# Optimization experiments

Measured on AMD Instinct MI355X. Metric: run time of the kernel, lower is better.

## Reference

```python
import jax, jax.numpy as jnp
import numpy as np

DEPTH_PARAM = 0.5
LENGTH_PENALTY = 1.5
LEVEL_COUNTS = [8, 32, 128, 512, 2048]  # nodes per tree level (branching factor 4)
BRANCH = 4
B = 4096


def _build_tree():
    counts = LEVEL_COUNTS
    D = len(counts)
    offsets = np.concatenate([[0], np.cumsum(counts)]).astype(np.int64)
    C = int(offsets[-1])
    path_ids = np.zeros((C, D), np.int32)   # ancestor matrix-id at each level (0-padded)
    path_len = np.zeros((C,), np.int32)     # depth of this class (= len of its path)
    sib_start = np.zeros((C, D), np.int32)  # start of contiguous sibling block at each level
    sib_size = np.zeros((C, D), np.int32)   # size of that block (valid_classes in torch code)
    for l in range(D):
        for k in range(counts[l]):
            gid = offsets[l] + k
            path_len[gid] = l + 1
            kk = k
            for a in range(l, -1, -1):
                path_ids[gid, a] = offsets[a] + kk
                if a == 0:
                    sib_start[gid, a] = 0
                    sib_size[gid, a] = counts[0]
                else:
                    sib_start[gid, a] = offsets[a] + (kk // BRANCH) * BRANCH
                    sib_size[gid, a] = BRANCH
                kk = kk // BRANCH
    return path_ids, path_len, sib_start, sib_size, C


def setup_inputs() -> dict:
    path_ids, path_len, sib_start, sib_size, C = _build_tree()
    key = jax.random.key(0)
    k1, k2 = jax.random.split(key)
    y_pred = jax.random.normal(k1, (B, C), dtype=jnp.float32)
    y_true = jax.random.normal(k2, (B, C), dtype=jnp.float32)  # only argmax is used
    rng = np.random.default_rng(0)
    counts = rng.integers(1, 1000, size=C).astype(np.float32)
    class_weights = jnp.asarray(counts.max() / counts, dtype=jnp.float32)
    return {
        "y_pred": y_pred,
        "y_true": y_true,
        "class_weights": class_weights,
        "path_ids": jnp.asarray(path_ids),
        "path_len": jnp.asarray(path_len),
        "sib_start": jnp.asarray(sib_start),
        "sib_size": jnp.asarray(sib_size),
    }


def reference(y_pred, y_true, class_weights, path_ids, path_len, sib_start, sib_size):
    Bsz, C = y_pred.shape
    D = path_ids.shape[1]
    pred_top = jnp.argmax(y_pred, axis=1)                    # [B]
    true_top = jnp.argmax(y_true, axis=1)                    # [B]
    len_p = path_len[pred_top]                               # [B]
    len_t = path_len[true_top]                               # [B]
    levels = jnp.arange(D)                                   # [D]
    # level in range(min(len(pred_path), len(true_path)))
    valid = levels[None, :] < jnp.minimum(len_p, len_t)[:, None]        # [B,D]
    height = (len_t[:, None] - levels[None, :] - 1).astype(y_pred.dtype)
    level_w = jnp.exp(-DEPTH_PARAM * height)                            # [B,D]
    t_ids = path_ids[true_top]                                          # [B,D]
    start = sib_start[true_top]                                         # [B,D]
    stop = start + sib_size[true_top]                                   # [B,D]
    cls = jnp.arange(C)
    mask = ((cls[None, None, :] >= start[:, :, None]) &
            (cls[None, None, :] < stop[:, :, None])).astype(y_pred.dtype)  # [B,D,C]
    # torch code multiplies logits by the 0/1 mask (NOT -inf masking)
    logits = y_pred[:, None, :] * mask                                  # [B,D,C]
    lse = jax.nn.logsumexp(logits, axis=-1)                             # [B,D]
    true_logit = jnp.take_along_axis(logits, t_ids[:, :, None], axis=-1)[..., 0]
    ce = lse - true_logit                                               # per-level cross entropy
    local = jnp.sum(jnp.where(valid, level_w * ce, 0.0), axis=1)        # [B]
    diff = jnp.abs(len_p - len_t).astype(y_pred.dtype)
    total = local * (LENGTH_PENALTY * diff) * class_weights[true_top]
    return jnp.mean(total)
```

## Files before the change

### kernel.cpp

```cpp
#include <hip/hip_runtime.h>
#include <hip/hip_bf16.h>
#include <float.h>

#define DEPTH_PARAM 0.5f
#define LENGTH_PENALTY 1.5f

__global__ __launch_bounds__(256) void hier_row_kernel(
    const float* __restrict__ y_pred,
    const float* __restrict__ y_true,
    const float* __restrict__ class_weights,
    const int* __restrict__ path_ids,
    const int* __restrict__ path_len,
    const int* __restrict__ sib_start,
    const int* __restrict__ sib_size,
    float* __restrict__ row_total,
    int C, int D, int Bsz)
{
    const int wid  = threadIdx.x >> 6;
    const int lane = threadIdx.x & 63;
    const int row  = blockIdx.x * 4 + wid;
    if (row >= Bsz) return;

    const float* __restrict__ yp = y_pred + (size_t)row * C;
    const float* __restrict__ yt = y_true + (size_t)row * C;

    float bp = -FLT_MAX; int bip = 0;
    float bt = -FLT_MAX; int bit_ = 0;
    const int C4 = C >> 2;
    const float4* __restrict__ yp4 = (const float4*)yp;
    const float4* __restrict__ yt4 = (const float4*)yt;

    for (int i = lane; i < C4; i += 64) {
        float4 v = yp4[i];
        float4 w = yt4[i];
        int base = i << 2;
        if (v.x > bp) { bp = v.x; bip = base + 0; }
        if (v.y > bp) { bp = v.y; bip = base + 1; }
        if (v.z > bp) { bp = v.z; bip = base + 2; }
        if (v.w > bp) { bp = v.w; bip = base + 3; }
        if (w.x > bt) { bt = w.x; bit_ = base + 0; }
        if (w.y > bt) { bt = w.y; bit_ = base + 1; }
        if (w.z > bt) { bt = w.z; bit_ = base + 2; }
        if (w.w > bt) { bt = w.w; bit_ = base + 3; }
    }
    for (int c = (C4 << 2) + lane; c < C; c += 64) {
        float v = yp[c]; if (v > bp) { bp = v; bip = c; }
        float w = yt[c]; if (w > bt) { bt = w; bit_ = c; }
    }

    for (int m = 1; m < 64; m <<= 1) {
        float ov = __shfl_xor(bp, m); int oi = __shfl_xor(bip, m);
        if (ov > bp || (ov == bp && oi < bip)) { bp = ov; bip = oi; }
        float ow = __shfl_xor(bt, m); int oj = __shfl_xor(bit_, m);
        if (ow > bt || (ow == bt && oj < bit_)) { bt = ow; bit_ = oj; }
    }
    const int pred_top = bip;
    const int true_top = bit_;

    const int lp = path_len[pred_top];
    const int lt = path_len[true_top];
    const int lmin = lp < lt ? lp : lt;

    float contrib = 0.0f;
    if (lane < lmin) {
        const int l   = lane;
        const int tix = path_ids[true_top * D + l];
        const int st  = sib_start[true_top * D + l];
        const int sz  = sib_size[true_top * D + l];
        float s = (float)(C - sz);
        for (int c = st; c < st + sz; c++) s += expf(yp[c]);
        const float ce = logf(s) - yp[tix];
        const float lw = expf(-DEPTH_PARAM * (float)(lt - l - 1));
        contrib = lw * ce;
    }
    for (int m = 1; m < 8; m <<= 1) contrib += __shfl_xor(contrib, m);

    if (lane == 0) {
        const float diff = fabsf((float)(lp - lt));
        row_total[row] = contrib * (LENGTH_PENALTY * diff) * class_weights[true_top];
    }
}

__global__ __launch_bounds__(256) void final_reduce_kernel(
    const float* __restrict__ row_total, float* __restrict__ out, int Bsz)
{
    const int tid = threadIdx.x;
    float s = 0.0f;
    for (int i = tid; i < Bsz; i += 256) s += row_total[i];
    for (int m = 1; m < 64; m <<= 1) s += __shfl_xor(s, m);

    __shared__ float sw[4];
    const int lane = tid & 63, wid = tid >> 6;
    if (lane == 0) sw[wid] = s;
    __syncthreads();
    if (tid == 0) {
        float t = sw[0] + sw[1] + sw[2] + sw[3];
        out[0] = t / (float)Bsz;
    }
}

extern "C" void kernel_launch(void* const* d_in, const int* in_sizes, int n_in,
                              void* d_out, int out_size, void* d_ws, size_t ws_size,
                              hipStream_t stream) {
    const float* y_pred        = (const float*)d_in[0];
    const float* y_true        = (const float*)d_in[1];
    const float* class_weights = (const float*)d_in[2];
    const int*   path_ids      = (const int*)d_in[3];
    const int*   path_len      = (const int*)d_in[4];
    const int*   sib_start     = (const int*)d_in[5];
    const int*   sib_size      = (const int*)d_in[6];
    float* out = (float*)d_out;
    float* row_total = (float*)d_ws;

    const int C = in_sizes[2];
    const int D = in_sizes[3] / C;
    const int B = in_sizes[0] / C;

    const int grid = (B + 3) / 4;
    hier_row_kernel<<<grid, 256, 0, stream>>>(
        y_pred, y_true, class_weights, path_ids, path_len,
        sib_start, sib_size, row_total, C, D, B);
    final_reduce_kernel<<<1, 256, 0, stream>>>(row_total, out, B);
}
```

Baseline: 122.9 us.

## Split each row across two waves and parallelize sibling logsumexp across lanes

Each row's argmax scan is now shared by two wavefronts, which merge their partial results through shared memory after a barrier. The grid doubles so each block handles two rows. The per-level sibling exp-sum is spread over 8 lanes per level and combined with shuffle reductions, replacing the serial per-lane loop. This adds more memory parallelism per row at the cost of a block barrier and twice as many blocks.

```diff
diff --git a/kernel.cpp b/kernel.cpp
--- a/kernel.cpp
+++ b/kernel.cpp
@@ -18,8 +18,9 @@
 {
     const int wid  = threadIdx.x >> 6;
     const int lane = threadIdx.x & 63;
-    const int row  = blockIdx.x * 4 + wid;
-    if (row >= Bsz) return;
+    const int half = wid & 1;
+    int row = blockIdx.x * 2 + (wid >> 1);
+    if (row >= Bsz) row = Bsz - 1;
 
     const float* __restrict__ yp = y_pred + (size_t)row * C;
     const float* __restrict__ yt = y_true + (size_t)row * C;
@@ -30,7 +31,7 @@
     const float4* __restrict__ yp4 = (const float4*)yp;
     const float4* __restrict__ yt4 = (const float4*)yt;
 
-    for (int i = lane; i < C4; i += 64) {
+    for (int i = half * 64 + lane; i < C4; i += 128) {
         float4 v = yp4[i];
         float4 w = yt4[i];
         int base = i << 2;
@@ -43,7 +44,7 @@
         if (w.z > bt) { bt = w.z; bit_ = base + 2; }
         if (w.w > bt) { bt = w.w; bit_ = base + 3; }
     }
-    for (int c = (C4 << 2) + lane; c < C; c += 64) {
+    for (int c = (C4 << 2) + half * 64 + lane; c < C; c += 128) {
         float v = yp[c]; if (v > bp) { bp = v; bip = c; }
         float w = yt[c]; if (w > bt) { bt = w; bit_ = c; }
     }
@@ -54,30 +55,57 @@
         float ow = __shfl_xor(bt, m); int oj = __shfl_xor(bit_, m);
         if (ow > bt || (ow == bt && oj < bit_)) { bt = ow; bit_ = oj; }
     }
-    const int pred_top = bip;
-    const int true_top = bit_;
 
-    const int lp = path_len[pred_top];
-    const int lt = path_len[true_top];
-    const int lmin = lp < lt ? lp : lt;
+    __shared__ float s_v[4][2];
+    __shared__ int   s_i[4][2];
+    if (lane == 0) {
+        s_v[wid][0] = bp;  s_i[wid][0] = bip;
+        s_v[wid][1] = bt;  s_i[wid][1] = bit_;
+    }
+    __syncthreads();
+    {
+        const int pw = wid ^ 1;
+        float ov = s_v[pw][0]; int oi = s_i[pw][0];
+        if (ov > bp || (ov == bp && oi < bip)) { bp = ov; bip = oi; }
+        float ow = s_v[pw][1]; int oj = s_i[pw][1];
+        if (ow > bt || (ow == bt && oj < bit_)) { bt = ow; bit_ = oj; }
+    }
 
-    float contrib = 0.0f;
-    if (lane < lmin) {
-        const int l   = lane;
-        const int tix = path_ids[true_top * D + l];
-        const int st  = sib_start[true_top * D + l];
-        const int sz  = sib_size[true_top * D + l];
-        float s = (float)(C - sz);
-        for (int c = st; c < st + sz; c++) s += expf(yp[c]);
-        const float ce = logf(s) - yp[tix];
-        const float lw = expf(-DEPTH_PARAM * (float)(lt - l - 1));
-        contrib = lw * ce;
-    }
-    for (int m = 1; m < 8; m <<= 1) contrib += __shfl_xor(contrib, m);
+    if (half == 0) {
+        const int pred_top = bip;
+        const int true_top = bit_;
+        const int lp = path_len[pred_top];
+        const int lt = path_len[true_top];
+        const int lmin = lp < lt ? lp : lt;
 
-    if (lane == 0) {
-        const float diff = fabsf((float)(lp - lt));
-        row_total[row] = contrib * (LENGTH_PENALTY * diff) * class_weights[true_top];
+        const int l = lane >> 3;
+        const int j = lane & 7;
+        float contrib = 0.0f;
+        float e = 0.0f;
+        int st = 0, sz = 0;
+        if (l < lmin) {
+            st = sib_start[true_top * D + l];
+            sz = sib_size[true_top * D + l];
+            if (j < sz) e = expf(yp[st + j]);
+        }
+        e += __shfl_xor(e, 1);
+        e += __shfl_xor(e, 2);
+        e += __shfl_xor(e, 4);
+        if (l < lmin && j == 0) {
+            const float s = e + (float)(C - sz);
+            const int tix = path_ids[true_top * D + l];
+            const float ce = logf(s) - yp[tix];
+            const float lw = expf(-DEPTH_PARAM * (float)(lt - l - 1));
+            contrib = lw * ce;
+        }
+        contrib += __shfl_xor(contrib, 8);
+        contrib += __shfl_xor(contrib, 16);
+        contrib += __shfl_xor(contrib, 32);
+
+        if (lane == 0) {
+            const float diff = fabsf((float)(lp - lt));
+            row_total[row] = contrib * (LENGTH_PENALTY * diff) * class_weights[true_top];
+        }
     }
 }
 
@@ -116,7 +144,7 @@
     const int D = in_sizes[3] / C;
     const int B = in_sizes[0] / C;
 
-    const int grid = (B + 3) / 4;
+    const int grid = (B + 1) / 2;
     hier_row_kernel<<<grid, 256, 0, stream>>>(
         y_pred, y_true, class_weights, path_ids, path_len,
         sib_start, sib_size, row_total, C, D, B);
```

New measurement: 120.2 us. -2.1%, faster.
